# Kernel tuning notes

Measured on AMD Instinct MI355X. Metric: run time of the kernel, lower is better.

## Reference

```python
import jax, jax.numpy as jnp
import numpy as np
from jax import lax

MAX_SCALE = 4
SCALES = [2 ** i for i in range(1, MAX_SCALE + 1)]  # [2,4,8,16]
EPS_K = 1e-7        # tf.keras.backend.epsilon()
BN_EPS = 1e-3       # keras BatchNormalization default epsilon


def sample_min_max_scaling(x):
    # per-sample min-max scaling over H, W, C
    mn = jnp.min(x, axis=(1, 2, 3), keepdims=True)
    mx = jnp.max(x, axis=(1, 2, 3), keepdims=True)
    return (x - mn) / (mx - mn + EPS_K)


def box_sum(x, r):
    # depthwise all-ones r x r conv, SAME padding (TF semantics)
    c = x.shape[-1]
    kernel = jnp.ones((r, r, 1, c), dtype=x.dtype)  # HWIO, depthwise
    return lax.conv_general_dilated(
        x, kernel, window_strides=(1, 1), padding='SAME',
        dimension_numbers=('NHWC', 'HWIO', 'NHWC'),
        feature_group_count=c)


def reference(x, gamma, beta, moving_mean, moving_var):
    x = sample_min_max_scaling(x)
    # multi-scale box-filter measures: [B,H,W,C,S]
    measures = jnp.stack([box_sum(x, r) for r in SCALES], axis=-1)
    # OLS slope of log(measure) vs log(scale) across the scale axis
    log_scales = jnp.log(jnp.asarray(SCALES, dtype=x.dtype))       # [S]
    log_measures = jnp.log(measures + EPS_K)                        # [B,H,W,C,S]
    mean_ls = jnp.mean(log_scales)
    mean_lm = jnp.mean(log_measures, axis=-1, keepdims=True)
    dls = log_scales - mean_ls                                      # [S]
    num = jnp.sum((log_measures - mean_lm) * dls, axis=-1)          # [B,H,W,C]
    den = jnp.sum(dls ** 2)
    alphas = num / den
    # BatchNormalization in inference mode (training=False)
    return (alphas - moving_mean) / jnp.sqrt(moving_var + BN_EPS) * gamma + beta


def setup_inputs() -> dict:
    key = jax.random.key(0)
    B, H, W, C = 16, 224, 224, 32
    x = jax.random.normal(key, (B, H, W, C), dtype=jnp.float32)
    return {
        'x': x,
        'gamma': jnp.ones((C,), jnp.float32),
        'beta': jnp.zeros((C,), jnp.float32),
        'moving_mean': jnp.zeros((C,), jnp.float32),
        'moving_var': jnp.ones((C,), jnp.float32),
    }
```

## Files before the change

### kernel.cpp

```cpp
#include <hip/hip_runtime.h>
#include <cstdint>

#define B_ 16
#define H_ 224
#define W_ 224
#define C_ 32
#define TS 32
#define RG 47
#define SR 48

__device__ __forceinline__ unsigned int enc_f(float f) {
    unsigned int u = __float_as_uint(f);
    return (u & 0x80000000u) ? ~u : (u | 0x80000000u);
}
__device__ __forceinline__ float dec_f(unsigned int u) {
    u = (u & 0x80000000u) ? (u & 0x7FFFFFFFu) : ~u;
    return __uint_as_float(u);
}

__global__ void init_ws(unsigned int* __restrict__ ws) {
    int t = threadIdx.x;
    if (t < 16) ws[t] = 0xFFFFFFFFu;
    else if (t < 32) ws[t] = 0u;
}

__global__ __launch_bounds__(256) void minmax_kernel(const float* __restrict__ x,
                                                     unsigned int* __restrict__ ws) {
    const int b = blockIdx.x;
    const int chunk = blockIdx.y;
    const int chunkElems = (H_ * W_ * C_) / 64;
    const float4* p = (const float4*)(x + (size_t)b * (H_ * W_ * C_) +
                                      (size_t)chunk * chunkElems);
    const int n4 = chunkElems / 4;
    float mn = 3.4e38f, mx = -3.4e38f;
    for (int i = threadIdx.x; i < n4; i += 256) {
        float4 v = p[i];
        mn = fminf(mn, fminf(fminf(v.x, v.y), fminf(v.z, v.w)));
        mx = fmaxf(mx, fmaxf(fmaxf(v.x, v.y), fmaxf(v.z, v.w)));
    }
#pragma unroll
    for (int off = 32; off > 0; off >>= 1) {
        mn = fminf(mn, __shfl_down(mn, off));
        mx = fmaxf(mx, __shfl_down(mx, off));
    }
    __shared__ float smn[4], smx[4];
    const int lane = threadIdx.x & 63, wv = threadIdx.x >> 6;
    if (lane == 0) { smn[wv] = mn; smx[wv] = mx; }
    __syncthreads();
    if (threadIdx.x == 0) {
        mn = fminf(fminf(smn[0], smn[1]), fminf(smn[2], smn[3]));
        mx = fmaxf(fmaxf(smx[0], smx[1]), fmaxf(smx[2], smx[3]));
        atomicMin(&ws[b], enc_f(mn));
        atomicMax(&ws[16 + b], enc_f(mx));
    }
}

template<int CTRL, int MASK>
__device__ __forceinline__ float dpp_add(float x) {
    int t = __builtin_amdgcn_update_dpp(0, (int)__float_as_uint(x),
                                        CTRL, MASK, 0xf, false);
    return x + __uint_as_float((unsigned)t);
}
template<int CTRL, int MASK>
__device__ __forceinline__ void dpp_step4(float4& v) {
    v.x = dpp_add<CTRL, MASK>(v.x);
    v.y = dpp_add<CTRL, MASK>(v.y);
    v.z = dpp_add<CTRL, MASK>(v.z);
    v.w = dpp_add<CTRL, MASK>(v.w);
}
__device__ __forceinline__ void hscan(float4& v) {
    dpp_step4<0x111, 0xf>(v);
    dpp_step4<0x112, 0xf>(v);
    dpp_step4<0x114, 0xf>(v);
    dpp_step4<0x118, 0xf>(v);
    dpp_step4<0x142, 0xa>(v);
    dpp_step4<0x143, 0xc>(v);
}

#define LG(v) __log2f(fmaxf((v), 0.0f) + 1e-7f)

#define BOX(S, o, sc, bx) {                                              \
        float4 q00 = S[hl + (o)][wl + (o)];                              \
        float4 q01 = S[hl + (o)][wl + (o) + (sc)];                       \
        float4 q10 = S[hl + (o) + (sc)][wl + (o)];                       \
        float4 q11 = S[hl + (o) + (sc)][wl + (o) + (sc)];                \
        bx.x = q11.x - q01.x - q10.x + q00.x;                            \
        bx.y = q11.y - q01.y - q10.y + q00.y;                            \
        bx.z = q11.z - q01.z - q10.z + q00.z;                            \
        bx.w = q11.w - q01.w - q10.w + q00.w; }

#define SC4(q) { q.x = (q.x - mn) * inv; q.y = (q.y - mn) * inv;         \
                 q.z = (q.z - mn) * inv; q.w = (q.w - mn) * inv; }

#define DOQUAD(qi, o4) {                                                 \
        const int ch0 = s * 16 + (qi) * 4;                               \
        const float4 (*S)[SR] = SAT[qi];                                 \
        float4 bx;                                                       \
        BOX(S, 7, 2, bx);                                                \
        float ax = -0.3f * LG(bx.x);                                     \
        float ay = -0.3f * LG(bx.y);                                     \
        float az = -0.3f * LG(bx.z);                                     \
        float aw = -0.3f * LG(bx.w);                                     \
        BOX(S, 6, 4, bx);                                                \
        ax -= 0.1f * LG(bx.x); ay -= 0.1f * LG(bx.y);                    \
        az -= 0.1f * LG(bx.z); aw -= 0.1f * LG(bx.w);                    \
        BOX(S, 4, 8, bx);                                                \
        ax += 0.1f * LG(bx.x); ay += 0.1f * LG(bx.y);                    \
        az += 0.1f * LG(bx.z); aw += 0.1f * LG(bx.w);                    \
        BOX(S, 0, 16, bx);                                               \
        ax += 0.3f * LG(bx.x); ay += 0.3f * LG(bx.y);                    \
        az += 0.3f * LG(bx.z); aw += 0.3f * LG(bx.w);                    \
        const float4 g4  = *(const float4*)(gamma + ch0);                \
        const float4 be4 = *(const float4*)(beta  + ch0);                \
        const float4 mm4 = *(const float4*)(mmean + ch0);                \
        const float4 mv4 = *(const float4*)(mvar  + ch0);                \
        o4.x = (ax - mm4.x) * (g4.x * rsqrtf(mv4.x + 1e-3f)) + be4.x;    \
        o4.y = (ay - mm4.y) * (g4.y * rsqrtf(mv4.y + 1e-3f)) + be4.y;    \
        o4.z = (az - mm4.z) * (g4.z * rsqrtf(mv4.z + 1e-3f)) + be4.z;    \
        o4.w = (aw - mm4.w) * (g4.w * rsqrtf(mv4.w + 1e-3f)) + be4.w; }

__global__ __launch_bounds__(1024, 4) void lss_kernel(
    const float* __restrict__ x,
    const float* __restrict__ gamma, const float* __restrict__ beta,
    const float* __restrict__ mmean, const float* __restrict__ mvar,
    const unsigned int* __restrict__ ws,
    float* __restrict__ out)
{
    __shared__ float4 SAT[4][SR][SR];

    const int bi = blockIdx.x;
    const int grp = bi >> 4, wi = bi & 15;
    const int s = (wi >> 3) & 1;
    const int tile = grp * 8 + (wi & 7);
    const int b = tile / 49;
    const int t2 = tile - b * 49;
    const int th0 = (t2 / 7) * TS;
    const int tw0 = (t2 % 7) * TS;
    const int tid = threadIdx.x;
    const int lane = tid & 63, wv = tid >> 6;

    const float mn = dec_f(ws[b]);
    const float mx = dec_f(ws[16 + b]);
    const float inv = 1.0f / (mx - mn + 1e-7f);

    const float* xb = x + (size_t)b * (H_ * W_ * C_);
    float* ob = out + (size_t)b * (H_ * W_ * C_);

#pragma unroll
    for (int p = 0; p < 3; ++p) {
        const int rr = wv + 16 * p;
        if (rr < RG) {
            const int gh = th0 - 7 + rr;
            const int gw = tw0 - 7 + lane;
            float4 q0 = make_float4(0.f, 0.f, 0.f, 0.f);
            float4 q1 = q0, q2 = q0, q3 = q0;
            if (lane < RG && gh >= 0 && gh < H_ && gw >= 0 && gw < W_) {
                const float4* p4 = (const float4*)(xb +
                    ((size_t)(gh * W_ + gw)) * C_ + s * 16);
                q0 = p4[0]; q1 = p4[1]; q2 = p4[2]; q3 = p4[3];
                SC4(q0); SC4(q1); SC4(q2); SC4(q3);
            }
            hscan(q0); hscan(q1); hscan(q2); hscan(q3);
            if (lane < RG) {
                SAT[0][rr][lane + 1] = q0;
                SAT[1][rr][lane + 1] = q1;
                SAT[2][rr][lane + 1] = q2;
                SAT[3][rr][lane + 1] = q3;
            } else if (lane == 63) {
                const float4 z = make_float4(0.f, 0.f, 0.f, 0.f);
                SAT[0][rr][0] = z; SAT[1][rr][0] = z;
                SAT[2][rr][0] = z; SAT[3][rr][0] = z;
            }
        }
    }
    __syncthreads();

    {
        const int q = tid >> 8;
        const int c = tid & 255;
        if (c < 192) {
            float* col = (float*)&SAT[q][0][0] + c;
            float accv = 0.f;
#pragma unroll
            for (int r = 0; r < SR; ++r) {
                const float t = (r < RG) ? col[r * 192] : 0.f;
                col[r * 192] = accv;
                accv += t;
            }
        }
    }
    __syncthreads();

    {
        const int hl = tid >> 5, wl = tid & 31;
        float4 o0, o1, o2, o3;
        DOQUAD(0, o0);
        DOQUAD(1, o1);
        DOQUAD(2, o2);
        DOQUAD(3, o3);
        float* dst = ob + ((size_t)((th0 + hl) * W_ + (tw0 + wl))) * C_ + s * 16;
        *(float4*)(dst + 0)  = o0;
        *(float4*)(dst + 4)  = o1;
        *(float4*)(dst + 8)  = o2;
        *(float4*)(dst + 12) = o3;
    }
}

extern "C" void kernel_launch(void* const* d_in, const int* in_sizes, int n_in,
                              void* d_out, int out_size, void* d_ws, size_t ws_size,
                              hipStream_t stream) {
    const float* x     = (const float*)d_in[0];
    const float* gamma = (const float*)d_in[1];
    const float* beta  = (const float*)d_in[2];
    const float* mmean = (const float*)d_in[3];
    const float* mvar  = (const float*)d_in[4];
    float* out = (float*)d_out;
    unsigned int* ws = (unsigned int*)d_ws;

    hipLaunchKernelGGL(init_ws, dim3(1), dim3(64), 0, stream, ws);
    hipLaunchKernelGGL(minmax_kernel, dim3(16, 64), dim3(256), 0, stream, x, ws);
    hipLaunchKernelGGL(lss_kernel, dim3(98 * 16), dim3(1024), 0, stream,
                       x, gamma, beta, mmean, mvar, ws, out);
}
```

Before: 283.7 us.

## Split LSS blocks to 8 channels, fold log terms, drop atomic init launch

The main kernel now handles 8 channels per block with 512 threads instead of 16 channels with 1024, which halves shared memory per block and doubles the grid. Each thread computes two output rows. The four per-scale log2 calls are folded into two via products of cubes, and the BN affine is folded into a single FMA. When the workspace is large enough, per-chunk min/max are written to slots and reduced inside the main kernel, removing the init kernel and the atomics. This adds a 64-entry reduction per block and a small risk of overflow or precision change from the products inside the logs.

Result: faster. 265.8 us (-6.3%).

```diff
diff --git a/kernel.cpp b/kernel.cpp
--- a/kernel.cpp
+++ b/kernel.cpp
@@ -24,15 +24,15 @@
     else if (t < 32) ws[t] = 0u;
 }
 
-__global__ __launch_bounds__(256) void minmax_kernel(const float* __restrict__ x,
-                                                     unsigned int* __restrict__ ws) {
+__device__ __forceinline__ void blk_minmax(const float* __restrict__ x,
+                                           float& mn, float& mx) {
     const int b = blockIdx.x;
     const int chunk = blockIdx.y;
     const int chunkElems = (H_ * W_ * C_) / 64;
     const float4* p = (const float4*)(x + (size_t)b * (H_ * W_ * C_) +
                                       (size_t)chunk * chunkElems);
     const int n4 = chunkElems / 4;
-    float mn = 3.4e38f, mx = -3.4e38f;
+    mn = 3.4e38f; mx = -3.4e38f;
     for (int i = threadIdx.x; i < n4; i += 256) {
         float4 v = p[i];
         mn = fminf(mn, fminf(fminf(v.x, v.y), fminf(v.z, v.w)));
@@ -47,11 +47,27 @@
     const int lane = threadIdx.x & 63, wv = threadIdx.x >> 6;
     if (lane == 0) { smn[wv] = mn; smx[wv] = mx; }
     __syncthreads();
+    mn = fminf(fminf(smn[0], smn[1]), fminf(smn[2], smn[3]));
+    mx = fmaxf(fmaxf(smx[0], smx[1]), fmaxf(smx[2], smx[3]));
+}
+
+__global__ __launch_bounds__(256) void minmax_slots(const float* __restrict__ x,
+                                                    float* __restrict__ wsf) {
+    float mn, mx;
+    blk_minmax(x, mn, mx);
     if (threadIdx.x == 0) {
-        mn = fminf(fminf(smn[0], smn[1]), fminf(smn[2], smn[3]));
-        mx = fmaxf(fmaxf(smx[0], smx[1]), fmaxf(smx[2], smx[3]));
-        atomicMin(&ws[b], enc_f(mn));
-        atomicMax(&ws[16 + b], enc_f(mx));
+        wsf[blockIdx.y * 16 + blockIdx.x] = mn;
+        wsf[1024 + blockIdx.y * 16 + blockIdx.x] = mx;
+    }
+}
+
+__global__ __launch_bounds__(256) void minmax_atomic(const float* __restrict__ x,
+                                                     unsigned int* __restrict__ ws) {
+    float mn, mx;
+    blk_minmax(x, mn, mx);
+    if (threadIdx.x == 0) {
+        atomicMin(&ws[blockIdx.x], enc_f(mn));
+        atomicMax(&ws[16 + blockIdx.x], enc_f(mx));
     }
 }
 
@@ -77,9 +93,9 @@
     dpp_step4<0x143, 0xc>(v);
 }
 
-#define LG(v) __log2f(fmaxf((v), 0.0f) + 1e-7f)
-
-#define BOX(S, o, sc, bx) {                                              \
+#define CL(a) (fmaxf((a), 0.0f) + 1e-7f)
+
+#define BOXD(S, o, sc, bx) {                                             \
         float4 q00 = S[hl + (o)][wl + (o)];                              \
         float4 q01 = S[hl + (o)][wl + (o) + (sc)];                       \
         float4 q10 = S[hl + (o) + (sc)][wl + (o)];                       \
@@ -89,96 +105,107 @@
         bx.z = q11.z - q01.z - q10.z + q00.z;                            \
         bx.w = q11.w - q01.w - q10.w + q00.w; }
 
-#define SC4(q) { q.x = (q.x - mn) * inv; q.y = (q.y - mn) * inv;         \
-                 q.z = (q.z - mn) * inv; q.w = (q.w - mn) * inv; }
+#define LSSCOMP(comp, OUT) {                                             \
+        const float tq = g4.comp * rsqrtf(mv4.comp + 1e-3f);             \
+        const float wq = 0.1f * tq;                                      \
+        const float oq = be4.comp - mm4.comp * tq;                       \
+        const float a2 = CL(b2.comp),  a4 = CL(b4.comp);                 \
+        const float a8 = CL(b8.comp),  a16 = CL(b16.comp);               \
+        const float Lq = __log2f(a16 * a16 * a16 * a8)                   \
+                       - __log2f(a2 * a2 * a2 * a4);                     \
+        OUT = fmaf(Lq, wq, oq); }
 
 #define DOQUAD(qi, o4) {                                                 \
-        const int ch0 = s * 16 + (qi) * 4;                               \
+        const int ch0 = chbase + (qi) * 4;                               \
         const float4 (*S)[SR] = SAT[qi];                                 \
-        float4 bx;                                                       \
-        BOX(S, 7, 2, bx);                                                \
-        float ax = -0.3f * LG(bx.x);                                     \
-        float ay = -0.3f * LG(bx.y);                                     \
-        float az = -0.3f * LG(bx.z);                                     \
-        float aw = -0.3f * LG(bx.w);                                     \
-        BOX(S, 6, 4, bx);                                                \
-        ax -= 0.1f * LG(bx.x); ay -= 0.1f * LG(bx.y);                    \
-        az -= 0.1f * LG(bx.z); aw -= 0.1f * LG(bx.w);                    \
-        BOX(S, 4, 8, bx);                                                \
-        ax += 0.1f * LG(bx.x); ay += 0.1f * LG(bx.y);                    \
-        az += 0.1f * LG(bx.z); aw += 0.1f * LG(bx.w);                    \
-        BOX(S, 0, 16, bx);                                               \
-        ax += 0.3f * LG(bx.x); ay += 0.3f * LG(bx.y);                    \
-        az += 0.3f * LG(bx.z); aw += 0.3f * LG(bx.w);                    \
+        float4 b2, b4, b8, b16;                                          \
+        BOXD(S, 7, 2, b2);                                               \
+        BOXD(S, 6, 4, b4);                                               \
+        BOXD(S, 4, 8, b8);                                               \
+        BOXD(S, 0, 16, b16);                                             \
         const float4 g4  = *(const float4*)(gamma + ch0);                \
         const float4 be4 = *(const float4*)(beta  + ch0);                \
         const float4 mm4 = *(const float4*)(mmean + ch0);                \
         const float4 mv4 = *(const float4*)(mvar  + ch0);                \
-        o4.x = (ax - mm4.x) * (g4.x * rsqrtf(mv4.x + 1e-3f)) + be4.x;    \
-        o4.y = (ay - mm4.y) * (g4.y * rsqrtf(mv4.y + 1e-3f)) + be4.y;    \
-        o4.z = (az - mm4.z) * (g4.z * rsqrtf(mv4.z + 1e-3f)) + be4.z;    \
-        o4.w = (aw - mm4.w) * (g4.w * rsqrtf(mv4.w + 1e-3f)) + be4.w; }
-
-__global__ __launch_bounds__(1024, 4) void lss_kernel(
+        LSSCOMP(x, o4.x); LSSCOMP(y, o4.y);                              \
+        LSSCOMP(z, o4.z); LSSCOMP(w, o4.w); }
+
+template<bool SLOTS>
+__global__ __launch_bounds__(512, 4) void lss_kernel(
     const float* __restrict__ x,
     const float* __restrict__ gamma, const float* __restrict__ beta,
     const float* __restrict__ mmean, const float* __restrict__ mvar,
     const unsigned int* __restrict__ ws,
     float* __restrict__ out)
 {
-    __shared__ float4 SAT[4][SR][SR];
+    __shared__ float4 SAT[2][SR][SR];
 
     const int bi = blockIdx.x;
-    const int grp = bi >> 4, wi = bi & 15;
-    const int s = (wi >> 3) & 1;
+    const int grp = bi >> 5, wi = bi & 31;
     const int tile = grp * 8 + (wi & 7);
+    const int s  = (wi >> 3) & 1;
+    const int qp = (wi >> 4) & 1;
     const int b = tile / 49;
     const int t2 = tile - b * 49;
     const int th0 = (t2 / 7) * TS;
     const int tw0 = (t2 % 7) * TS;
     const int tid = threadIdx.x;
     const int lane = tid & 63, wv = tid >> 6;
-
-    const float mn = dec_f(ws[b]);
-    const float mx = dec_f(ws[16 + b]);
+    const int chbase = s * 16 + qp * 8;
+
+    float mn, mx;
+    if (SLOTS) {
+        const float* wsf = (const float*)ws;
+        mn = 3.4e38f; mx = -3.4e38f;
+#pragma unroll
+        for (int i = 0; i < 64; ++i) {
+            mn = fminf(mn, wsf[i * 16 + b]);
+            mx = fmaxf(mx, wsf[1024 + i * 16 + b]);
+        }
+    } else {
+        mn = dec_f(ws[b]);
+        mx = dec_f(ws[16 + b]);
+    }
     const float inv = 1.0f / (mx - mn + 1e-7f);
+    const float nmi = -mn * inv;
 
     const float* xb = x + (size_t)b * (H_ * W_ * C_);
     float* ob = out + (size_t)b * (H_ * W_ * C_);
 
 #pragma unroll
-    for (int p = 0; p < 3; ++p) {
-        const int rr = wv + 16 * p;
+    for (int p = 0; p < 6; ++p) {
+        const int rr = wv + 8 * p;
         if (rr < RG) {
             const int gh = th0 - 7 + rr;
             const int gw = tw0 - 7 + lane;
             float4 q0 = make_float4(0.f, 0.f, 0.f, 0.f);
-            float4 q1 = q0, q2 = q0, q3 = q0;
+            float4 q1 = q0;
             if (lane < RG && gh >= 0 && gh < H_ && gw >= 0 && gw < W_) {
                 const float4* p4 = (const float4*)(xb +
-                    ((size_t)(gh * W_ + gw)) * C_ + s * 16);
-                q0 = p4[0]; q1 = p4[1]; q2 = p4[2]; q3 = p4[3];
-                SC4(q0); SC4(q1); SC4(q2); SC4(q3);
+                    ((size_t)(gh * W_ + gw)) * C_ + chbase);
+                q0 = p4[0]; q1 = p4[1];
+                q0.x = fmaf(q0.x, inv, nmi); q0.y = fmaf(q0.y, inv, nmi);
+                q0.z = fmaf(q0.z, inv, nmi); q0.w = fmaf(q0.w, inv, nmi);
+                q1.x = fmaf(q1.x, inv, nmi); q1.y = fmaf(q1.y, inv, nmi);
+                q1.z = fmaf(q1.z, inv, nmi); q1.w = fmaf(q1.w, inv, nmi);
             }
-            hscan(q0); hscan(q1); hscan(q2); hscan(q3);
+            hscan(q0); hscan(q1);
             if (lane < RG) {
                 SAT[0][rr][lane + 1] = q0;
                 SAT[1][rr][lane + 1] = q1;
-                SAT[2][rr][lane + 1] = q2;
-                SAT[3][rr][lane + 1] = q3;
             } else if (lane == 63) {
                 const float4 z = make_float4(0.f, 0.f, 0.f, 0.f);
                 SAT[0][rr][0] = z; SAT[1][rr][0] = z;
-                SAT[2][rr][0] = z; SAT[3][rr][0] = z;
             }
         }
     }
     __syncthreads();
 
     {
-        const int q = tid >> 8;
-        const int c = tid & 255;
-        if (c < 192) {
+        int q = -1, c = 0;
+        if (tid < 192)      { q = 0; c = tid; }
+        else if (tid < 384) { q = 1; c = tid - 192; }
+        if (q >= 0) {
             float* col = (float*)&SAT[q][0][0] + c;
             float accv = 0.f;
 #pragma unroll
@@ -192,17 +219,18 @@
     __syncthreads();
 
     {
-        const int hl = tid >> 5, wl = tid & 31;
-        float4 o0, o1, o2, o3;
-        DOQUAD(0, o0);
-        DOQUAD(1, o1);
-        DOQUAD(2, o2);
-        DOQUAD(3, o3);
-        float* dst = ob + ((size_t)((th0 + hl) * W_ + (tw0 + wl))) * C_ + s * 16;
-        *(float4*)(dst + 0)  = o0;
-        *(float4*)(dst + 4)  = o1;
-        *(float4*)(dst + 8)  = o2;
-        *(float4*)(dst + 12) = o3;
+        const int wl = tid & 31;
+        const int hl0 = tid >> 5;
+#pragma unroll
+        for (int pp = 0; pp < 2; ++pp) {
+            const int hl = hl0 + pp * 16;
+            float4 o0, o1;
+            DOQUAD(0, o0);
+            DOQUAD(1, o1);
+            float* dst = ob + ((size_t)((th0 + hl) * W_ + (tw0 + wl))) * C_ + chbase;
+            *(float4*)(dst + 0) = o0;
+            *(float4*)(dst + 4) = o1;
+        }
     }
 }
 
@@ -217,8 +245,15 @@
     float* out = (float*)d_out;
     unsigned int* ws = (unsigned int*)d_ws;
 
-    hipLaunchKernelGGL(init_ws, dim3(1), dim3(64), 0, stream, ws);
-    hipLaunchKernelGGL(minmax_kernel, dim3(16, 64), dim3(256), 0, stream, x, ws);
-    hipLaunchKernelGGL(lss_kernel, dim3(98 * 16), dim3(1024), 0, stream,
-                       x, gamma, beta, mmean, mvar, ws, out);
-}
+    if (ws_size >= 8192) {
+        hipLaunchKernelGGL(minmax_slots, dim3(16, 64), dim3(256), 0, stream,
+                           x, (float*)ws);
+        hipLaunchKernelGGL((lss_kernel<true>), dim3(98 * 32), dim3(512), 0, stream,
+                           x, gamma, beta, mmean, mvar, ws, out);
+    } else {
+        hipLaunchKernelGGL(init_ws, dim3(1), dim3(64), 0, stream, ws);
+        hipLaunchKernelGGL(minmax_atomic, dim3(16, 64), dim3(256), 0, stream, x, ws);
+        hipLaunchKernelGGL((lss_kernel<false>), dim3(98 * 32), dim3(512), 0, stream,
+                           x, gamma, beta, mmean, mvar, ws, out);
+    }
+}
```
